# Performance work log

Hardware: AMD Instinct MI355X
Metric: run time of the kernel (lower is better)

The kernel has to match this reference:

```python
import jax, jax.numpy as jnp
import numpy as np

EMBED_DIM = 1024
LATENT = 512
HEADS = 8
HEAD_DIM = EMBED_DIM // HEADS        # 128
LAT_HD = LATENT // HEADS             # 64
EPS = 1e-5


def _layernorm(x, gamma, beta):
    mu = jnp.mean(x, axis=-1, keepdims=True)
    var = jnp.mean(jnp.square(x - mu), axis=-1, keepdims=True)
    return (x - mu) * jax.lax.rsqrt(var + EPS) * gamma + beta


def setup_inputs() -> dict:
    key = jax.random.key(0)
    ks = jax.random.split(key, 12)
    B, N, M = 8, 8192, 256
    s_in = 1.0 / np.sqrt(EMBED_DIM)
    return {
        "input_tokens": jax.random.normal(ks[0], (B, N, EMBED_DIM), jnp.float32),
        "query_tokens": jax.random.normal(ks[1], (B, M, EMBED_DIM), jnp.float32),
        # Linear weights stored as [in, out] so y = x @ W + b
        "q_w": jax.random.normal(ks[2], (EMBED_DIM, LATENT), jnp.float32) * s_in,
        "q_b": jnp.zeros((LATENT,), jnp.float32),
        "q_g": jnp.ones((LATENT,), jnp.float32),
        "q_beta": jnp.zeros((LATENT,), jnp.float32),
        "k_w": jax.random.normal(ks[3], (EMBED_DIM, LATENT), jnp.float32) * s_in,
        "k_b": jnp.zeros((LATENT,), jnp.float32),
        "k_g": jnp.ones((LATENT,), jnp.float32),
        "k_beta": jnp.zeros((LATENT,), jnp.float32),
        "v_w": jax.random.normal(ks[4], (EMBED_DIM, EMBED_DIM), jnp.float32) * s_in,
        "v_b": jnp.zeros((EMBED_DIM,), jnp.float32),
        "v_g": jnp.ones((EMBED_DIM,), jnp.float32),
        "v_beta": jnp.zeros((EMBED_DIM,), jnp.float32),
        "proj_w": jax.random.normal(ks[5], (EMBED_DIM, EMBED_DIM), jnp.float32) * s_in,
        "proj_b": jnp.zeros((EMBED_DIM,), jnp.float32),
    }


def reference(input_tokens, query_tokens, q_w, q_b, q_g, q_beta,
              k_w, k_b, k_g, k_beta, v_w, v_b, v_g, v_beta,
              proj_w, proj_b):
    B, N, C = input_tokens.shape
    M = query_tokens.shape[1]
    # projections + layernorms
    q = _layernorm(query_tokens @ q_w + q_b, q_g, q_beta)   # [B,M,LATENT]
    k = _layernorm(input_tokens @ k_w + k_b, k_g, k_beta)   # [B,N,LATENT]
    v = _layernorm(input_tokens @ v_w + v_b, v_g, v_beta)   # [B,N,C]
    # split heads: q,k -> [B,H,*,LAT_HD]; v -> [B,H,N,HEAD_DIM]
    q = q.reshape(B, M, HEADS, LAT_HD).transpose(0, 2, 1, 3)
    k = k.reshape(B, N, HEADS, LAT_HD).transpose(0, 2, 1, 3)
    v = v.reshape(B, N, HEADS, HEAD_DIM).transpose(0, 2, 1, 3)
    # softmax Q over latent head dim; softmax K^T over token dim N
    q = jax.nn.softmax(q, axis=-1)                 # [B,H,M,LAT_HD]
    kT = jax.nn.softmax(k.transpose(0, 1, 3, 2), axis=-1)  # [B,H,LAT_HD,N]
    kv = jnp.einsum('bhln,bhnd->bhld', kT, v)      # [B,H,LAT_HD,HEAD_DIM]
    out = jnp.einsum('bhml,bhld->bhmd', q, kv)     # [B,H,M,HEAD_DIM]
    out = out.transpose(0, 2, 1, 3).reshape(B, M, C)
    return out @ proj_w + proj_b
```

## Files before the change

kernel.cpp:

```cpp
#include <hip/hip_runtime.h>
#include <hip/hip_fp16.h>

typedef _Float16 f16;
typedef _Float16 f16x8 __attribute__((ext_vector_type(8)));
typedef _Float16 f16x4 __attribute__((ext_vector_type(4)));
typedef float f32x4 __attribute__((ext_vector_type(4)));

#define LN_EPS 1e-5f

typedef __attribute__((address_space(1))) unsigned int as1_u32;
typedef __attribute__((address_space(3))) unsigned int as3_u32;

__device__ __forceinline__ void gload_lds16(const void* g, void* l) {
    __builtin_amdgcn_global_load_lds((as1_u32*)g, (as3_u32*)l, 16, 0, 0);
}

__device__ __forceinline__ f32x4 mfma16(f16x8 a, f16x8 b, f32x4 c) {
    return __builtin_amdgcn_mfma_f32_16x16x32_f16(a, b, c, 0, 0, 0);
}


__global__ void k_cvt4(const float4* __restrict__ in, f16x4* __restrict__ out, int n4) {
    int i = blockIdx.x * blockDim.x + threadIdx.x;
    int st = gridDim.x * blockDim.x;
    for (; i < n4; i += st) {
        float4 v = in[i];
        f16x4 o;
        o.x = (f16)v.x; o.y = (f16)v.y; o.z = (f16)v.z; o.w = (f16)v.w;
        out[i] = o;
    }
}

__global__ __launch_bounds__(256) void k_transpose_cvt(const float* __restrict__ W,
                                                       f16* __restrict__ WT, int Nw) {
    __shared__ float t[32][33];
    int n0 = blockIdx.x * 32, k0 = blockIdx.y * 32;
    int tx = threadIdx.x & 31, ty = threadIdx.x >> 5;
#pragma unroll
    for (int i = 0; i < 32; i += 8)
        t[ty + i][tx] = W[(size_t)(k0 + ty + i) * Nw + n0 + tx];
    __syncthreads();
#pragma unroll
    for (int i = 0; i < 32; i += 8)
        WT[(size_t)(n0 + ty + i) * 1024 + k0 + tx] = (f16)t[tx][ty + i];
}


template <bool OUTF32>
__global__ __launch_bounds__(256, 2) void k_gemm(const f16* __restrict__ A,
                                                 const f16* __restrict__ Bt,
                                                 void* __restrict__ Cout, int Ncols, int Kd,
                                                 const float* __restrict__ bias1,
                                                 const float* __restrict__ bias2, int bsplit) {
    __shared__ f16 smem[16384];
    const int tid = threadIdx.x, lane = tid & 63, wave = tid >> 6;
    const int m0 = blockIdx.y * 128, n0 = blockIdx.x * 128;
    const size_t ldb = (size_t)Kd * 2;
    f32x4 acc[4][4] = {};

    const int rA = wave * 8 + (lane >> 3);
    const int slot = (lane & 7) * 16;
    const char* Ab = (const char*)A + (size_t)(m0 + rA) * ldb + slot;
    const char* Bb = (const char*)Bt + (size_t)(n0 + rA) * ldb + slot;
    char* lA = (char*)smem + wave * 1024;
    char* lB = (char*)smem + 16384 + wave * 1024;

    const int wm = (wave & 1) * 64, wn = (wave >> 1) * 64;

    for (int k0 = 0; k0 < Kd; k0 += 64) {
#pragma unroll
        for (int i = 0; i < 4; i++) {
            gload_lds16(Ab + (size_t)k0 * 2 + (size_t)i * 32 * ldb, lA + i * 4096);
            gload_lds16(Bb + (size_t)k0 * 2 + (size_t)i * 32 * ldb, lB + i * 4096);
        }
        __syncthreads();
#pragma unroll
        for (int kk = 0; kk < 64; kk += 32) {
            const int kb = (kk + (lane >> 4) * 8) * 2;
            f16x8 af[4], bf[4];
#pragma unroll
            for (int mi = 0; mi < 4; mi++)
                af[mi] = *(const f16x8*)((const char*)smem + (wm + mi * 16 + (lane & 15)) * 128 + kb);
#pragma unroll
            for (int ni = 0; ni < 4; ni++)
                bf[ni] = *(const f16x8*)((const char*)smem + 16384 + (wn + ni * 16 + (lane & 15)) * 128 + kb);
#pragma unroll
            for (int mi = 0; mi < 4; mi++)
#pragma unroll
                for (int ni = 0; ni < 4; ni++)
                    acc[mi][ni] = mfma16(af[mi], bf[ni], acc[mi][ni]);
        }
        __syncthreads();
    }

    if (!OUTF32) {
        f16* Ct = smem;
#pragma unroll
        for (int mi = 0; mi < 4; mi++) {
#pragma unroll
            for (int ni = 0; ni < 4; ni++) {
                const int r = wm + mi * 16 + (lane >> 4) * 4;
                const int c = wn + ni * 16 + (lane & 15);
                const int cg = n0 + c;
                const float bv = (cg < bsplit) ? bias1[cg] : bias2[cg - bsplit];
#pragma unroll
                for (int j = 0; j < 4; j++) Ct[(r + j) * 128 + c] = (f16)(acc[mi][ni][j] + bv);
            }
        }
        __syncthreads();
        f16* Cg = (f16*)Cout;
        const int r = tid >> 1, half = tid & 1;
        const f16* src = Ct + r * 128 + half * 64;
        f16* dst = Cg + (size_t)(m0 + r) * Ncols + n0 + half * 64;
#pragma unroll
        for (int i = 0; i < 8; i++) *(f16x8*)(dst + i * 8) = *(const f16x8*)(src + i * 8);
    } else {
        float* Cg = (float*)Cout;
#pragma unroll
        for (int mi = 0; mi < 4; mi++) {
#pragma unroll
            for (int ni = 0; ni < 4; ni++) {
                const int r = wm + mi * 16 + (lane >> 4) * 4;
                const int c = wn + ni * 16 + (lane & 15);
                const int cg = n0 + c;
                const float bv = (cg < bsplit) ? bias1[cg] : bias2[cg - bsplit];
#pragma unroll
                for (int j = 0; j < 4; j++)
                    Cg[(size_t)(m0 + r + j) * Ncols + cg] = acc[mi][ni][j] + bv;
            }
        }
    }
}


__global__ __launch_bounds__(192) void k_rowstats(const f16* __restrict__ Ckv,
                                                  float* __restrict__ stats) {
    const int row = blockIdx.x, t = threadIdx.x;
    const f16x8 v = ((const f16x8*)(Ckv + (size_t)row * 1536))[t];
    float s = 0.f, s2 = 0.f;
#pragma unroll
    for (int j = 0; j < 8; j++) {
        float x = (float)v[j];
        s += x;
        s2 += x * x;
    }
#pragma unroll
    for (int off = 32; off; off >>= 1) {
        s += __shfl_xor(s, off);
        s2 += __shfl_xor(s2, off);
    }
    __shared__ float red[4];
    const int wave = t >> 6;
    if ((t & 63) == 0 && wave) {
        red[wave * 2 - 2] = s;
        red[wave * 2 - 1] = s2;
    }
    __syncthreads();
    float* st = stats + (size_t)row * 4;
    if (t == 0) {
        const float mu = s * (1.0f / 512.0f);
        const float var = s2 * (1.0f / 512.0f) - mu * mu;
        st[0] = mu;
        st[1] = rsqrtf(var + LN_EPS);
    } else if (t == 64) {
        const float ss = s + red[2], ss2 = s2 + red[3];
        const float mu = ss * (1.0f / 1024.0f);
        const float var = ss2 * (1.0f / 1024.0f) - mu * mu;
        st[2] = mu;
        st[3] = rsqrtf(var + LN_EPS);
    }
}


__global__ __launch_bounds__(256) void k_colstats1(const f16* __restrict__ Ckv,
                                                   const float4* __restrict__ stats,
                                                   const float* __restrict__ kg,
                                                   const float* __restrict__ kb,
                                                   float* __restrict__ pm, float* __restrict__ ps) {
    const int b = blockIdx.y, slab = blockIdx.x, t = threadIdx.x;
    const int c0 = t * 2;
    const float g0 = kg[c0], g1 = kg[c0 + 1], e0 = kb[c0], e1 = kb[c0 + 1];
    const size_t r0 = (size_t)b * 8192 + slab * 256;
    float m0 = -1e30f, m1 = -1e30f;
    for (int r = 0; r < 256; r++) {
        const float4 st = stats[r0 + r];
        union { unsigned u; f16 h[2]; } w;
        w.u = *(const unsigned*)(Ckv + (r0 + r) * 1536 + c0);
        const float z0 = ((float)w.h[0] - st.x) * st.y * g0 + e0;
        const float z1 = ((float)w.h[1] - st.x) * st.y * g1 + e1;
        m0 = fmaxf(m0, z0);
        m1 = fmaxf(m1, z1);
    }
    float s0 = 0.f, s1 = 0.f;
    for (int r = 0; r < 256; r++) {
        const float4 st = stats[r0 + r];
        union { unsigned u; f16 h[2]; } w;
        w.u = *(const unsigned*)(Ckv + (r0 + r) * 1536 + c0);
        const float z0 = ((float)w.h[0] - st.x) * st.y * g0 + e0;
        const float z1 = ((float)w.h[1] - st.x) * st.y * g1 + e1;
        s0 += __expf(z0 - m0);
        s1 += __expf(z1 - m1);
    }
    const int o = (b * 32 + slab) * 512 + c0;
    pm[o] = m0; pm[o + 1] = m1;
    ps[o] = s0; ps[o + 1] = s1;
}

__global__ void k_colstats2(const float* __restrict__ pm, const float* __restrict__ ps,
                            float* __restrict__ Mx, float* __restrict__ invZ) {
    const int idx = blockIdx.x * 256 + threadIdx.x;
    const int b = idx >> 9, c = idx & 511;
    float M = -1e30f;
    for (int s = 0; s < 32; s++) M = fmaxf(M, pm[(b * 32 + s) * 512 + c]);
    float S = 0.f;
    for (int s = 0; s < 32; s++) S += ps[(b * 32 + s) * 512 + c] * __expf(pm[(b * 32 + s) * 512 + c] - M);
    Mx[idx] = M;
    invZ[idx] = 1.0f / S;
}


__global__ __launch_bounds__(256, 2) void k_kv(const f16* __restrict__ Ckv,
                                               const float4* __restrict__ stats,
                                               const float* __restrict__ kg,
                                               const float* __restrict__ kbe,
                                               const float* __restrict__ vg,
                                               const float* __restrict__ vbe,
                                               const float* __restrict__ Mx,
                                               float* __restrict__ kvpart) {
    __shared__ f16 As[64 * 64];
    __shared__ f16 Vs[128 * 64];
    __shared__ float cgk[64], cbk[64], cmx[64], cgv[128], cbv[128];
    const int split = blockIdx.x, bh = blockIdx.y;
    const int b = bh >> 3, h = bh & 7;
    const int tid = threadIdx.x, lane = tid & 63, wave = tid >> 6;
    if (tid < 64) {
        cgk[tid] = kg[h * 64 + tid];
        cbk[tid] = kbe[h * 64 + tid];
        cmx[tid] = Mx[b * 512 + h * 64 + tid];
    }
    if (tid < 128) {
        cgv[tid] = vg[h * 128 + tid];
        cbv[tid] = vbe[h * 128 + tid];
    }
    __syncthreads();
    f32x4 acc[8] = {};
    const size_t base = (size_t)b * 8192 + split * 1024;
    for (int t0 = 0; t0 < 1024; t0 += 64) {
        {
            const int g = tid & 7, p = tid >> 3;
            const size_t row = base + t0 + 2 * p;
            const f16x8 x0 = *(const f16x8*)(Ckv + row * 1536 + h * 64 + g * 8);
            const f16x8 x1 = *(const f16x8*)(Ckv + (row + 1) * 1536 + h * 64 + g * 8);
            const float4 s0 = stats[row], s1 = stats[row + 1];
#pragma unroll
            for (int j = 0; j < 8; j++) {
                const int c = g * 8 + j;
                const float z0 = ((float)x0[j] - s0.x) * s0.y * cgk[c] + cbk[c] - cmx[c];
                const float z1 = ((float)x1[j] - s1.x) * s1.y * cgk[c] + cbk[c] - cmx[c];
                union { unsigned u; f16 h2[2]; } pk;
                pk.h2[0] = (f16)__expf(z0);
                pk.h2[1] = (f16)__expf(z1);
                *(unsigned*)((char*)As + c * 128 + 4 * p) = pk.u;
            }
        }
#pragma unroll
        for (int sub = 0; sub < 2; sub++) {
            const int idx = tid + sub * 256;
            const int g = idx & 15, p = idx >> 4;
            const size_t row = base + t0 + 2 * p;
            const f16x8 x0 = *(const f16x8*)(Ckv + row * 1536 + 512 + h * 128 + g * 8);
            const f16x8 x1 = *(const f16x8*)(Ckv + (row + 1) * 1536 + 512 + h * 128 + g * 8);
            const float4 s0 = stats[row], s1 = stats[row + 1];
#pragma unroll
            for (int j = 0; j < 8; j++) {
                const int d = g * 8 + j;
                const float z0 = ((float)x0[j] - s0.z) * s0.w * cgv[d] + cbv[d];
                const float z1 = ((float)x1[j] - s1.z) * s1.w * cgv[d] + cbv[d];
                union { unsigned u; f16 h2[2]; } pk;
                pk.h2[0] = (f16)z0;
                pk.h2[1] = (f16)z1;
                *(unsigned*)((char*)Vs + d * 128 + 4 * p) = pk.u;
            }
        }
        __syncthreads();
#pragma unroll
        for (int kk = 0; kk < 64; kk += 32) {
            const int kb2 = (kk + (lane >> 4) * 8) * 2;
            const f16x8 af = *(const f16x8*)((const char*)As + (wave * 16 + (lane & 15)) * 128 + kb2);
#pragma unroll
            for (int ni = 0; ni < 8; ni++) {
                const f16x8 bf = *(const f16x8*)((const char*)Vs + (ni * 16 + (lane & 15)) * 128 + kb2);
                acc[ni] = mfma16(af, bf, acc[ni]);
            }
        }
        __syncthreads();
    }
    float* out = kvpart + ((size_t)split * 64 + bh) * 8192;
    const int l = wave * 16 + (lane >> 4) * 4;
#pragma unroll
    for (int ni = 0; ni < 8; ni++) {
        const int d = ni * 16 + (lane & 15);
#pragma unroll
        for (int j = 0; j < 4; j++) out[(l + j) * 128 + d] = acc[ni][j];
    }
}

__global__ void k_kvreduce(const float* __restrict__ kvpart, const float* __restrict__ invZ,
                           f16* __restrict__ kvT) {
    const int idx = blockIdx.x * 256 + threadIdx.x;
    const int d = idx & 127, l = (idx >> 7) & 63, bh = idx >> 13;
    const int b = bh >> 3, h = bh & 7;
    float s = 0.f;
#pragma unroll
    for (int sp = 0; sp < 8; sp++) s += kvpart[((size_t)sp * 64 + bh) * 8192 + l * 128 + d];
    s *= invZ[b * 512 + h * 64 + l];
    kvT[((size_t)bh * 128 + d) * 64 + l] = (f16)s;
}


__global__ __launch_bounds__(512) void k_qsm(const f16* __restrict__ qlin,
                                             const float* __restrict__ qg,
                                             const float* __restrict__ qbeta,
                                             f16* __restrict__ qsm) {
    const int row = blockIdx.x, t = threadIdx.x;
    const float x = (float)qlin[(size_t)row * 512 + t];
    float s = x, s2 = x * x;
#pragma unroll
    for (int off = 32; off; off >>= 1) {
        s += __shfl_xor(s, off);
        s2 += __shfl_xor(s2, off);
    }
    __shared__ float rs[16];
    const int wave = t >> 6, lane = t & 63;
    if (lane == 0) {
        rs[wave] = s;
        rs[8 + wave] = s2;
    }
    __syncthreads();
    float S = 0.f, S2 = 0.f;
#pragma unroll
    for (int w = 0; w < 8; w++) {
        S += rs[w];
        S2 += rs[8 + w];
    }
    const float mu = S * (1.0f / 512.0f);
    const float var = S2 * (1.0f / 512.0f) - mu * mu;
    const float z = (x - mu) * rsqrtf(var + LN_EPS) * qg[t] + qbeta[t];
    float m = z;
#pragma unroll
    for (int off = 32; off; off >>= 1) m = fmaxf(m, __shfl_xor(m, off));
    const float e = __expf(z - m);
    float se = e;
#pragma unroll
    for (int off = 32; off; off >>= 1) se += __shfl_xor(se, off);
    qsm[(size_t)row * 512 + t] = (f16)(e / se);
}


__global__ __launch_bounds__(256) void k_qkv(const f16* __restrict__ qsm,
                                             const f16* __restrict__ kvT,
                                             f16* __restrict__ omid) {
    const int ms = blockIdx.x, bh = blockIdx.y;
    const int b = bh >> 3, h = bh & 7;
    const int tid = threadIdx.x, lane = tid & 63, wave = tid >> 6;
    const int mr = ms * 64 + wave * 16;
    f32x4 acc[8] = {};
    const f16* Ab = qsm + (size_t)(b * 256 + mr + (lane & 15)) * 512 + h * 64;
    const f16* Bb = kvT + (size_t)bh * 8192;
#pragma unroll
    for (int kk = 0; kk < 64; kk += 32) {
        const int k = kk + (lane >> 4) * 8;
        const f16x8 af = *(const f16x8*)(Ab + k);
#pragma unroll
        for (int ni = 0; ni < 8; ni++) {
            const f16x8 bf = *(const f16x8*)(Bb + (ni * 16 + (lane & 15)) * 64 + k);
            acc[ni] = mfma16(af, bf, acc[ni]);
        }
    }
    const int r = b * 256 + mr + (lane >> 4) * 4;
#pragma unroll
    for (int ni = 0; ni < 8; ni++) {
        const int d = h * 128 + ni * 16 + (lane & 15);
#pragma unroll
        for (int j = 0; j < 4; j++) omid[(size_t)(r + j) * 1024 + d] = (f16)acc[ni][j];
    }
}


extern "C" void kernel_launch(void* const* d_in, const int* in_sizes, int n_in,
                              void* d_out, int out_size, void* d_ws, size_t ws_size,
                              hipStream_t stream) {
    const float* input  = (const float*)d_in[0];
    const float* query  = (const float*)d_in[1];
    const float* q_w    = (const float*)d_in[2];
    const float* q_b    = (const float*)d_in[3];
    const float* q_g    = (const float*)d_in[4];
    const float* q_beta = (const float*)d_in[5];
    const float* k_w    = (const float*)d_in[6];
    const float* k_b    = (const float*)d_in[7];
    const float* k_g    = (const float*)d_in[8];
    const float* k_beta = (const float*)d_in[9];
    const float* v_w    = (const float*)d_in[10];
    const float* v_b    = (const float*)d_in[11];
    const float* v_g    = (const float*)d_in[12];
    const float* v_beta = (const float*)d_in[13];
    const float* proj_w = (const float*)d_in[14];
    const float* proj_b = (const float*)d_in[15];

    char* ws = (char*)d_ws;
    size_t off = 0;
    auto alloc = [&](size_t bytes) {
        char* p = ws + off;
        off += (bytes + 255) & ~(size_t)255;
        return p;
    };
    f16*   A16    = (f16*)alloc((size_t)67108864 * 2);
    f16*   Q16    = (f16*)alloc((size_t)2097152 * 2);
    f16*   BkvT   = (f16*)alloc((size_t)1536 * 1024 * 2);
    f16*   qwT    = (f16*)alloc((size_t)512 * 1024 * 2);
    f16*   pwT    = (f16*)alloc((size_t)1024 * 1024 * 2);
    f16*   Ckv    = (f16*)alloc((size_t)65536 * 1536 * 2);
    float* stats  = (float*)alloc((size_t)65536 * 16);
    float* pm     = (float*)alloc((size_t)8 * 32 * 512 * 4);
    float* ps     = (float*)alloc((size_t)8 * 32 * 512 * 4);
    float* Mx     = (float*)alloc((size_t)8 * 512 * 4);
    float* invZ   = (float*)alloc((size_t)8 * 512 * 4);
    f16*   qlin   = (f16*)alloc((size_t)2048 * 512 * 2);
    f16*   qsm    = (f16*)alloc((size_t)2048 * 512 * 2);
    float* kvpart = (float*)alloc((size_t)8 * 64 * 64 * 128 * 4);
    f16*   kvT    = (f16*)alloc((size_t)64 * 128 * 64 * 2);
    f16*   omid   = (f16*)alloc((size_t)2048 * 1024 * 2);
    (void)ws_size; (void)in_sizes; (void)n_in; (void)out_size;

    k_cvt4<<<2048, 256, 0, stream>>>((const float4*)input, (f16x4*)A16, 16777216);
    k_cvt4<<<512, 256, 0, stream>>>((const float4*)query, (f16x4*)Q16, 524288);
    k_transpose_cvt<<<dim3(16, 32), 256, 0, stream>>>(k_w, BkvT, 512);
    k_transpose_cvt<<<dim3(32, 32), 256, 0, stream>>>(v_w, BkvT + (size_t)512 * 1024, 1024);
    k_transpose_cvt<<<dim3(16, 32), 256, 0, stream>>>(q_w, qwT, 512);
    k_transpose_cvt<<<dim3(32, 32), 256, 0, stream>>>(proj_w, pwT, 1024);

    k_gemm<false><<<dim3(12, 512), 256, 0, stream>>>(A16, BkvT, Ckv, 1536, 1024, k_b, v_b, 512);

    k_rowstats<<<65536, 192, 0, stream>>>(Ckv, stats);

    k_colstats1<<<dim3(32, 8), 256, 0, stream>>>(Ckv, (const float4*)stats, k_g, k_beta, pm, ps);
    k_colstats2<<<16, 256, 0, stream>>>(pm, ps, Mx, invZ);

    k_kv<<<dim3(8, 64), 256, 0, stream>>>(Ckv, (const float4*)stats, k_g, k_beta, v_g, v_beta, Mx, kvpart);
    k_kvreduce<<<2048, 256, 0, stream>>>(kvpart, invZ, kvT);

    k_gemm<false><<<dim3(4, 16), 256, 0, stream>>>(Q16, qwT, qlin, 512, 1024, q_b, q_b, 512);
    k_qsm<<<2048, 512, 0, stream>>>(qlin, q_g, q_beta, qsm);
    k_qkv<<<dim3(4, 64), 256, 0, stream>>>(qsm, kvT, omid);
    k_gemm<true><<<dim3(8, 16), 256, 0, stream>>>(omid, pwT, d_out, 1024, 1024, proj_b, proj_b, 2048);
}
```

Measured before the change: 983.7 us.

## Add 256x256 LDS-swizzled GEMM for KV projection, fuse setup kernels, widen colstats grid

Replaces the 128x128 KV projection GEMM with a 512-thread 256x256 tile kernel. It uses 128KB of dynamic LDS with double-buffered direct-to-LDS loads, XOR swizzling, block-index swizzling for L2 locality, and an LDS-staged coalesced epilogue. It also merges the two f32->f16 conversions into one launch and the four weight transposes into one launch. The column-stats grid grows from 32 to 128 slabs per batch for more parallelism. The big tile raises per-CU data reuse but limits occupancy and leans on careful vmcnt handling.

New measurement: 897.9 us. 1.1x faster.

```diff
diff --git a/kernel.cpp b/kernel.cpp
--- a/kernel.cpp
+++ b/kernel.cpp
@@ -20,22 +20,36 @@
 }
 
 
-__global__ void k_cvt4(const float4* __restrict__ in, f16x4* __restrict__ out, int n4) {
+__global__ void k_cvt_dual(const float4* __restrict__ in0, const float4* __restrict__ in1,
+                           f16x4* __restrict__ out0, f16x4* __restrict__ out1,
+                           int nsplit, int ntot) {
     int i = blockIdx.x * blockDim.x + threadIdx.x;
     int st = gridDim.x * blockDim.x;
-    for (; i < n4; i += st) {
-        float4 v = in[i];
+    for (; i < ntot; i += st) {
+        const bool lo = i < nsplit;
+        const float4 v = lo ? in0[i] : in1[i - nsplit];
         f16x4 o;
         o.x = (f16)v.x; o.y = (f16)v.y; o.z = (f16)v.z; o.w = (f16)v.w;
-        out[i] = o;
-    }
-}
-
-__global__ __launch_bounds__(256) void k_transpose_cvt(const float* __restrict__ W,
-                                                       f16* __restrict__ WT, int Nw) {
+        if (lo) out0[i] = o; else out1[i - nsplit] = o;
+    }
+}
+
+__global__ __launch_bounds__(256) void k_transpose_all(const float* __restrict__ kw,
+                                                       const float* __restrict__ vw,
+                                                       const float* __restrict__ qw,
+                                                       const float* __restrict__ pw,
+                                                       f16* __restrict__ BkvT,
+                                                       f16* __restrict__ qwT,
+                                                       f16* __restrict__ pwT) {
     __shared__ float t[32][33];
-    int n0 = blockIdx.x * 32, k0 = blockIdx.y * 32;
-    int tx = threadIdx.x & 31, ty = threadIdx.x >> 5;
+    const int x = blockIdx.x;
+    const float* W; f16* WT; int Nw, nt0;
+    if (x < 16)      { W = kw; WT = BkvT;                     Nw = 512;  nt0 = x; }
+    else if (x < 48) { W = vw; WT = BkvT + (size_t)512 * 1024; Nw = 1024; nt0 = x - 16; }
+    else if (x < 64) { W = qw; WT = qwT;                      Nw = 512;  nt0 = x - 48; }
+    else             { W = pw; WT = pwT;                      Nw = 1024; nt0 = x - 64; }
+    const int n0 = nt0 * 32, k0 = blockIdx.y * 32;
+    const int tx = threadIdx.x & 31, ty = threadIdx.x >> 5;
 #pragma unroll
     for (int i = 0; i < 32; i += 8)
         t[ty + i][tx] = W[(size_t)(k0 + ty + i) * Nw + n0 + tx];
@@ -43,6 +57,118 @@
 #pragma unroll
     for (int i = 0; i < 32; i += 8)
         WT[(size_t)(n0 + ty + i) * 1024 + k0 + tx] = (f16)t[tx][ty + i];
+}
+
+
+__global__ __launch_bounds__(512, 2) void k_gemm256(const f16* __restrict__ A,
+                                                    const f16* __restrict__ Bt,
+                                                    f16* __restrict__ C,
+                                                    const float* __restrict__ bias1,
+                                                    const float* __restrict__ bias2) {
+    extern __shared__ char lds[];
+    const int tid = threadIdx.x, lane = tid & 63, w = tid >> 6;
+    const int wr = w >> 2, wc = w & 3;
+    const int lane15 = lane & 15, l4 = lane >> 4;
+
+    const int swz = ((int)blockIdx.x & 7) * 192 + ((int)blockIdx.x >> 3);
+    const int bx = swz % 6, by = swz / 6;
+    const size_t m0 = (size_t)by * 256, n0g = (size_t)bx * 256;
+
+    const int lrow = lane >> 3;
+    const int slot = (lane & 7) ^ lrow;
+    const int rw = w * 32;
+    const f16* gA = A + (m0 + rw + lrow) * 1024 + slot * 8;
+    const f16* gB = Bt + (n0g + rw + lrow) * 1024 + slot * 8;
+    const int ldsw = rw * 128;
+
+    const int sf = l4 ^ (lane15 & 7);
+    const int offA = (wr * 128 + lane15) * 128 + sf * 16;
+    const int offB = (wc * 64 + lane15) * 128 + sf * 16;
+
+    f32x4 acc[8][4] = {};
+
+#define STAGE(t, bsel)                                                          \
+    {                                                                           \
+        const int k0s = (t) * 64;                                               \
+        char* dA = lds + ((bsel) << 15) + ldsw;                                 \
+        char* dB = lds + 65536 + ((bsel) << 15) + ldsw;                         \
+        _Pragma("unroll")                                                       \
+        for (int i = 0; i < 4; i++) {                                           \
+            gload_lds16(gA + (size_t)i * 8192 + k0s, dA + i * 1024);            \
+            gload_lds16(gB + (size_t)i * 8192 + k0s, dB + i * 1024);            \
+        }                                                                       \
+    }
+
+    STAGE(0, 0)
+    STAGE(1, 1)
+    asm volatile("s_waitcnt vmcnt(8)" ::: "memory");
+    __builtin_amdgcn_s_barrier();
+
+    for (int t = 0; t < 16; ++t) {
+        const int bsel = t & 1;
+        const char* pA = lds + (bsel << 15);
+        const char* pB = lds + 65536 + (bsel << 15);
+#pragma unroll
+        for (int q = 0; q < 4; ++q) {
+            const int mh = (q >> 1) * 4, nh = (q & 1) * 2;
+            f16x8 af[4][2], bf[2][2];
+#pragma unroll
+            for (int mi = 0; mi < 4; mi++)
+#pragma unroll
+                for (int kk = 0; kk < 2; kk++)
+                    af[mi][kk] = *(const f16x8*)(pA + ((offA + (mh + mi) * 2048) ^ (kk << 6)));
+#pragma unroll
+            for (int ni = 0; ni < 2; ni++)
+#pragma unroll
+                for (int kk = 0; kk < 2; kk++)
+                    bf[ni][kk] = *(const f16x8*)(pB + ((offB + (nh + ni) * 2048) ^ (kk << 6)));
+            __builtin_amdgcn_s_setprio(1);
+#pragma unroll
+            for (int mi = 0; mi < 4; mi++)
+#pragma unroll
+                for (int ni = 0; ni < 2; ni++)
+#pragma unroll
+                    for (int kk = 0; kk < 2; kk++)
+                        acc[mh + mi][nh + ni] =
+                            mfma16(af[mi][kk], bf[ni][kk], acc[mh + mi][nh + ni]);
+            __builtin_amdgcn_s_setprio(0);
+        }
+        __builtin_amdgcn_s_barrier();
+        if (t < 14) {
+            STAGE(t + 2, bsel)
+            asm volatile("s_waitcnt vmcnt(8)" ::: "memory");
+        } else {
+            asm volatile("s_waitcnt vmcnt(0)" ::: "memory");
+        }
+        __builtin_amdgcn_s_barrier();
+    }
+#undef STAGE
+
+    {
+        f16* Ct = (f16*)lds;
+#pragma unroll
+        for (int mi = 0; mi < 8; mi++) {
+#pragma unroll
+            for (int ni = 0; ni < 4; ni++) {
+                const int row = wr * 128 + mi * 16 + l4 * 4;
+                const int col = wc * 64 + ni * 16 + lane15;
+                const int cg = (int)n0g + col;
+                const float bv = (cg < 512) ? bias1[cg] : bias2[cg - 512];
+#pragma unroll
+                for (int j = 0; j < 4; j++)
+                    Ct[(row + j) * 256 + col] = (f16)(acc[mi][ni][j] + bv);
+            }
+        }
+        asm volatile("s_waitcnt lgkmcnt(0)" ::: "memory");
+        __builtin_amdgcn_s_barrier();
+#pragma unroll
+        for (int it = 0; it < 16; it++) {
+            const int flat = it * 512 + tid;
+            const int row = flat >> 5;
+            const int ce = (flat & 31) * 8;
+            *(f16x8*)(C + (m0 + row) * 1536 + n0g + ce) = *(const f16x8*)(Ct + row * 256 + ce);
+        }
+    }
 }
 
 
@@ -180,9 +306,9 @@
     const int b = blockIdx.y, slab = blockIdx.x, t = threadIdx.x;
     const int c0 = t * 2;
     const float g0 = kg[c0], g1 = kg[c0 + 1], e0 = kb[c0], e1 = kb[c0 + 1];
-    const size_t r0 = (size_t)b * 8192 + slab * 256;
+    const size_t r0 = (size_t)b * 8192 + slab * 64;
     float m0 = -1e30f, m1 = -1e30f;
-    for (int r = 0; r < 256; r++) {
+    for (int r = 0; r < 64; r++) {
         const float4 st = stats[r0 + r];
         union { unsigned u; f16 h[2]; } w;
         w.u = *(const unsigned*)(Ckv + (r0 + r) * 1536 + c0);
@@ -192,7 +318,7 @@
         m1 = fmaxf(m1, z1);
     }
     float s0 = 0.f, s1 = 0.f;
-    for (int r = 0; r < 256; r++) {
+    for (int r = 0; r < 64; r++) {
         const float4 st = stats[r0 + r];
         union { unsigned u; f16 h[2]; } w;
         w.u = *(const unsigned*)(Ckv + (r0 + r) * 1536 + c0);
@@ -201,7 +327,7 @@
         s0 += __expf(z0 - m0);
         s1 += __expf(z1 - m1);
     }
-    const int o = (b * 32 + slab) * 512 + c0;
+    const int o = (b * 128 + slab) * 512 + c0;
     pm[o] = m0; pm[o + 1] = m1;
     ps[o] = s0; ps[o + 1] = s1;
 }
@@ -211,9 +337,9 @@
     const int idx = blockIdx.x * 256 + threadIdx.x;
     const int b = idx >> 9, c = idx & 511;
     float M = -1e30f;
-    for (int s = 0; s < 32; s++) M = fmaxf(M, pm[(b * 32 + s) * 512 + c]);
+    for (int s = 0; s < 128; s++) M = fmaxf(M, pm[(b * 128 + s) * 512 + c]);
     float S = 0.f;
-    for (int s = 0; s < 32; s++) S += ps[(b * 32 + s) * 512 + c] * __expf(pm[(b * 32 + s) * 512 + c] - M);
+    for (int s = 0; s < 128; s++) S += ps[(b * 128 + s) * 512 + c] * __expf(pm[(b * 128 + s) * 512 + c] - M);
     Mx[idx] = M;
     invZ[idx] = 1.0f / S;
 }
@@ -421,8 +547,8 @@
     f16*   pwT    = (f16*)alloc((size_t)1024 * 1024 * 2);
     f16*   Ckv    = (f16*)alloc((size_t)65536 * 1536 * 2);
     float* stats  = (float*)alloc((size_t)65536 * 16);
-    float* pm     = (float*)alloc((size_t)8 * 32 * 512 * 4);
-    float* ps     = (float*)alloc((size_t)8 * 32 * 512 * 4);
+    float* pm     = (float*)alloc((size_t)8 * 128 * 512 * 4);
+    float* ps     = (float*)alloc((size_t)8 * 128 * 512 * 4);
     float* Mx     = (float*)alloc((size_t)8 * 512 * 4);
     float* invZ   = (float*)alloc((size_t)8 * 512 * 4);
     f16*   qlin   = (f16*)alloc((size_t)2048 * 512 * 2);
@@ -432,18 +558,18 @@
     f16*   omid   = (f16*)alloc((size_t)2048 * 1024 * 2);
     (void)ws_size; (void)in_sizes; (void)n_in; (void)out_size;
 
-    k_cvt4<<<2048, 256, 0, stream>>>((const float4*)input, (f16x4*)A16, 16777216);
-    k_cvt4<<<512, 256, 0, stream>>>((const float4*)query, (f16x4*)Q16, 524288);
-    k_transpose_cvt<<<dim3(16, 32), 256, 0, stream>>>(k_w, BkvT, 512);
-    k_transpose_cvt<<<dim3(32, 32), 256, 0, stream>>>(v_w, BkvT + (size_t)512 * 1024, 1024);
-    k_transpose_cvt<<<dim3(16, 32), 256, 0, stream>>>(q_w, qwT, 512);
-    k_transpose_cvt<<<dim3(32, 32), 256, 0, stream>>>(proj_w, pwT, 1024);
-
-    k_gemm<false><<<dim3(12, 512), 256, 0, stream>>>(A16, BkvT, Ckv, 1536, 1024, k_b, v_b, 512);
+    hipFuncSetAttribute(reinterpret_cast<const void*>(k_gemm256),
+                        hipFuncAttributeMaxDynamicSharedMemorySize, 131072);
+
+    k_cvt_dual<<<2048, 256, 0, stream>>>((const float4*)input, (const float4*)query,
+                                         (f16x4*)A16, (f16x4*)Q16, 16777216, 17301504);
+    k_transpose_all<<<dim3(96, 32), 256, 0, stream>>>(k_w, v_w, q_w, proj_w, BkvT, qwT, pwT);
+
+    k_gemm256<<<1536, 512, 131072, stream>>>(A16, BkvT, Ckv, k_b, v_b);
 
     k_rowstats<<<65536, 192, 0, stream>>>(Ckv, stats);
 
-    k_colstats1<<<dim3(32, 8), 256, 0, stream>>>(Ckv, (const float4*)stats, k_g, k_beta, pm, ps);
+    k_colstats1<<<dim3(128, 8), 256, 0, stream>>>(Ckv, (const float4*)stats, k_g, k_beta, pm, ps);
     k_colstats2<<<16, 256, 0, stream>>>(pm, ps, Mx, invZ);
 
     k_kv<<<dim3(8, 64), 256, 0, stream>>>(Ckv, (const float4*)stats, k_g, k_beta, v_g, v_beta, Mx, kvpart);
```
